# Performance work log

Measured on AMD Instinct MI355X. Metric: run time of the kernel, lower is better.

## Reference

```python
import jax, jax.numpy as jnp
import numpy as np

N = 50000   # nodes
E = 800000  # edges (avg degree 16)
D = 128     # in_channels == num_hidden_channels


def setup_inputs() -> dict:
    key = jax.random.key(0)
    ks = jax.random.split(key, 8)
    embs = jax.random.normal(ks[0], (N, D), dtype=jnp.float32)
    edge_index0 = jax.random.randint(ks[1], (2, E), 0, N)
    edge_index1 = jax.random.randint(ks[2], (2, E), 0, N)
    s = 1.0 / np.sqrt(D)  # torch Linear default init bound
    Wl0 = jax.random.uniform(ks[3], (D, D), jnp.float32, -s, s)
    Wr0 = jax.random.uniform(ks[4], (D, D), jnp.float32, -s, s)
    bl0 = jax.random.uniform(ks[5], (D,), jnp.float32, -s, s)
    Wl1 = jax.random.uniform(ks[6], (D, D), jnp.float32, -s, s)
    Wr1 = jax.random.uniform(ks[7], (D, D), jnp.float32, -s, s)
    bl1 = jnp.zeros((D,), jnp.float32)
    return {"embs": embs, "edge_index0": edge_index0, "edge_index1": edge_index1,
            "Wl0": Wl0, "bl0": bl0, "Wr0": Wr0, "Wl1": Wl1, "bl1": bl1, "Wr1": Wr1}


def sage_conv(x, edge_index, Wl, bl, Wr):
    # PyG SAGEConv, aggr='mean': out = lin_l(mean_{j->i} x_j) + lin_r(x_i)
    src, dst = edge_index[0], edge_index[1]
    msg = x[src]  # [E, D] gather of source-node features
    agg = jax.ops.segment_sum(msg, dst, num_segments=x.shape[0])            # [N, D]
    cnt = jax.ops.segment_sum(jnp.ones((src.shape[0],), x.dtype), dst,
                              num_segments=x.shape[0])                      # [N]
    mean = agg / jnp.maximum(cnt, 1.0)[:, None]  # isolated nodes -> 0 (scatter_mean)
    return mean @ Wl + bl + x @ Wr


def reference(embs, edge_index0, edge_index1, Wl0, bl0, Wr0, Wl1, bl1, Wr1):
    # outer layer 0 (not last) -> conv, dropout (eval: identity), exact GELU
    x = sage_conv(embs, edge_index0, Wl0, bl0, Wr0)
    x = jax.nn.gelu(x, approximate=False)
    # outer layer 1 (last) -> conv only
    x = sage_conv(x, edge_index1, Wl1, bl1, Wr1)
    return x
```

## Files before the change

### kernel.cpp

```cpp
#include <hip/hip_runtime.h>
#include <math.h>

#define D 128
#define BKT_SHIFT 8
#define CHUNK 4096
#define CAP 5120
#define CAPC 56

typedef __attribute__((ext_vector_type(8))) short bf8;
typedef __attribute__((ext_vector_type(4))) float f4;

__device__ __forceinline__ float b2f(ushort u) {
    union { uint i; float f; } x; x.i = ((uint)u) << 16; return x.f;
}
__device__ __forceinline__ ushort f2b(float f) {
    union { float f; uint i; } x; x.f = f;
    uint i = x.i;
    i += 0x7fffu + ((i >> 16) & 1u);
    return (ushort)(i >> 16);
}

__global__ __launch_bounds__(256)
void prep_scatter(const int* __restrict__ ei0, const int* __restrict__ ei1, int E,
                  int ncnk, int* __restrict__ chunkcnt, uint* __restrict__ tmpf,
                  const float* __restrict__ embs, ushort* __restrict__ xb, long n4,
                  const float* __restrict__ Wl0, const float* __restrict__ Wr0,
                  const float* __restrict__ Wl1, const float* __restrict__ Wr1,
                  ushort* __restrict__ WTsw) {
    __shared__ char smem[3088 + CHUNK * 4];
    const int t = threadIdx.x;

    if (blockIdx.y == 2) {
        if (blockIdx.x < 4) {
            const float* Wsrc = blockIdx.x == 0 ? Wl0 : blockIdx.x == 1 ? Wr0
                               : blockIdx.x == 2 ? Wl1 : Wr1;
            ushort* dstm = WTsw + (size_t)blockIdx.x * D * D;
            ushort (*tile)[33] = (ushort(*)[33])smem;
            const int r  = t >> 3;
            const int c0 = (t & 7) * 4;
            for (int tt = 0; tt < 16; ++tt) {
                int ti = tt >> 2, tj = tt & 3;
                float4 v = *(const float4*)(Wsrc + (ti * 32 + r) * D + tj * 32 + c0);
                tile[r][c0 + 0] = f2b(v.x);
                tile[r][c0 + 1] = f2b(v.y);
                tile[r][c0 + 2] = f2b(v.z);
                tile[r][c0 + 3] = f2b(v.w);
                __syncthreads();
                int row = tj * 32 + r;
                int off = row * 256 + (ti * 32 + c0) * 2;
                int doff = off ^ ((row & 7) << 4);
                ushort4 o = { tile[c0 + 0][r], tile[c0 + 1][r],
                              tile[c0 + 2][r], tile[c0 + 3][r] };
                *(ushort4*)((char*)dstm + doff) = o;
                __syncthreads();
            }
            return;
        }
        long i = (long)(blockIdx.x - 4) * 256 + t;
        long stride = (long)(gridDim.x - 4) * 256;
        for (; i < n4; i += stride) {
            float4 v = ((const float4*)embs)[i];
            ushort4 o = { f2b(v.x), f2b(v.y), f2b(v.z), f2b(v.w) };
            ((ushort4*)xb)[i] = o;
        }
        return;
    }

    int* lhist  = (int*)smem;
    int* lstart = (int*)(smem + 1024);
    int* lcur   = (int*)(smem + 2048);
    int* ws     = (int*)(smem + 3072);
    uint* sw    = (uint*)(smem + 3088);
    const int layer = blockIdx.y;
    const int* ei = layer ? ei1 : ei0;
    uint* tp = tmpf + ((size_t)layer * ncnk + blockIdx.x) * 256 * CAPC;
    const int e0 = blockIdx.x * CHUNK;
    const int cnt = min(CHUNK, E - e0);
    lhist[t] = 0;
    __syncthreads();
    for (int i = t; i < cnt; i += 256)
        atomicAdd(&lhist[ei[E + e0 + i] >> BKT_SHIFT], 1);
    __syncthreads();
    {
        int lane = t & 63, wid = t >> 6;
        int v = lhist[t];
        int incl = v;
        #pragma unroll
        for (int o = 1; o < 64; o <<= 1) { int u = __shfl_up(incl, o); if (lane >= o) incl += u; }
        if (lane == 63) ws[wid] = incl;
        __syncthreads();
        int wb = 0;
        #pragma unroll
        for (int w = 0; w < 3; ++w) if (w < wid) wb += ws[w];
        int excl = incl - v + wb;
        lstart[t] = excl;
        lcur[t] = excl;
    }
    __syncthreads();
    for (int i = t; i < cnt; i += 256) {
        int s = ei[e0 + i];
        int d = ei[E + e0 + i];
        int r = atomicAdd(&lcur[d >> BKT_SHIFT], 1);
        sw[r] = ((uint)d << 16) | (uint)s;
    }
    __syncthreads();
    chunkcnt[((size_t)layer * ncnk + blockIdx.x) * 256 + t] = min(lhist[t], CAPC);
    for (int i = t; i < cnt; i += 256) {
        uint w = sw[i];
        int b = w >> 24;
        int o = i - lstart[b];
        if (o < CAPC) tp[b * CAPC + o] = w;
    }
}

__global__ __launch_bounds__(256)
void exact_place(const uint* __restrict__ tmpf, const int* __restrict__ chunkcnt,
                 int ncnk,
                 int* __restrict__ o0, int* __restrict__ o1,
                 int* __restrict__ d0, int* __restrict__ d1,
                 ushort* __restrict__ s0, ushort* __restrict__ s1, int N) {
    const int layer = blockIdx.y;
    const int b = blockIdx.x;
    int* offs = layer ? o1 : o0;
    int* deg  = layer ? d1 : d0;
    ushort* srcs = layer ? s1 : s0;
    __shared__ int lh[256], lc[256], ccnt[256];
    __shared__ int ws[4];
    const int t = threadIdx.x;
    const int lane = t & 63, wid = t >> 6;
    const int node0 = b << BKT_SHIFT;
    const int bstart = b * CAP;

    lh[t] = 0;
    ccnt[t] = (t < ncnk) ? chunkcnt[((size_t)layer * ncnk + t) * 256 + b] : 0;
    __syncthreads();

    for (int c = wid; c < ncnk; c += 4) {
        int cc = ccnt[c];
        if (lane < cc) {
            uint w = tmpf[(((size_t)layer * ncnk + c) * 256 + b) * CAPC + lane];
            atomicAdd(&lh[(w >> 16) & 255], 1);
        }
    }
    __syncthreads();
    {
        int v = lh[t];
        int incl = v;
        #pragma unroll
        for (int o = 1; o < 64; o <<= 1) { int u = __shfl_up(incl, o); if (lane >= o) incl += u; }
        if (lane == 63) ws[wid] = incl;
        __syncthreads();
        int wb = 0;
        #pragma unroll
        for (int w = 0; w < 3; ++w) if (w < wid) wb += ws[w];
        int excl = incl - v + wb;
        int node = node0 + t;
        if (node < N) { offs[node] = bstart + excl; deg[node] = v; }
        lc[t] = bstart + excl;
    }
    __syncthreads();
    for (int c = wid; c < ncnk; c += 4) {
        int cc = ccnt[c];
        if (lane < cc) {
            uint w = tmpf[(((size_t)layer * ncnk + c) * 256 + b) * CAPC + lane];
            int p = atomicAdd(&lc[(w >> 16) & 255], 1);
            srcs[p] = (ushort)(w & 0xffff);
        }
    }
}

__global__ void gather_mean_b(const ushort* __restrict__ xb, const ushort* __restrict__ srcs,
                              const int* __restrict__ offs, const int* __restrict__ deg,
                              ushort* __restrict__ meanb, int N) {
    int node = blockIdx.x * (blockDim.x >> 6) + (threadIdx.x >> 6);
    if (node >= N) return;
    int lane = threadIdx.x & 63;
    int g = lane >> 4;
    int c = (lane & 15) * 8;
    int beg = offs[node], dc = deg[node];
    int end = beg + dc;
    float a[8] = {0.f, 0.f, 0.f, 0.f, 0.f, 0.f, 0.f, 0.f};
    for (int base = beg + g; base < end; base += 16) {
        int i0 = base, i1 = base + 4, i2 = base + 8, i3 = base + 12;
        int s0 = srcs[i0 < end ? i0 : beg];
        int s1 = srcs[i1 < end ? i1 : beg];
        int s2 = srcs[i2 < end ? i2 : beg];
        int s3 = srcs[i3 < end ? i3 : beg];
        float w0 = i0 < end ? 1.f : 0.f;
        float w1 = i1 < end ? 1.f : 0.f;
        float w2 = i2 < end ? 1.f : 0.f;
        float w3 = i3 < end ? 1.f : 0.f;
        bf8 v0 = *(const bf8*)(xb + (long)s0 * D + c);
        bf8 v1 = *(const bf8*)(xb + (long)s1 * D + c);
        bf8 v2 = *(const bf8*)(xb + (long)s2 * D + c);
        bf8 v3 = *(const bf8*)(xb + (long)s3 * D + c);
        #pragma unroll
        for (int q = 0; q < 8; ++q) {
            a[q] = fmaf(w0, b2f((ushort)v0[q]), a[q]);
            a[q] = fmaf(w1, b2f((ushort)v1[q]), a[q]);
            a[q] = fmaf(w2, b2f((ushort)v2[q]), a[q]);
            a[q] = fmaf(w3, b2f((ushort)v3[q]), a[q]);
        }
    }
    #pragma unroll
    for (int q = 0; q < 8; ++q) {
        a[q] += __shfl_xor(a[q], 16);
        a[q] += __shfl_xor(a[q], 32);
    }
    if (g == 0) {
        float inv = dc > 0 ? 1.0f / (float)dc : 0.0f;
        bf8 o;
        #pragma unroll
        for (int q = 0; q < 8; ++q) o[q] = (short)f2b(a[q] * inv);
        *(bf8*)(meanb + (long)node * D + c) = o;
    }
}

template <int ACT>
__global__ __launch_bounds__(256, 2)
void gemm_mfma(const ushort* __restrict__ meanb, const ushort* __restrict__ xb,
               const ushort* __restrict__ WTsw,
               const float* __restrict__ bias, float* __restrict__ outf,
               ushort* __restrict__ outb, int N) {
    __shared__ ushort sW[2 * D * D];
    const int t = threadIdx.x;
    const int lane = t & 63;
    const int wid  = t >> 6;

    {
        const char* src = (const char*)WTsw;
        char* dst = (char*)sW;
        #pragma unroll
        for (int i = 0; i < 16; ++i) {
            int off = i * 4096 + t * 16;
            __builtin_amdgcn_global_load_lds(
                (const __attribute__((address_space(1))) unsigned int*)(src + off),
                (__attribute__((address_space(3))) unsigned int*)(dst + off),
                16, 0, 0);
        }
    }

    const int r0   = blockIdx.x * 128 + wid * 32;
    const int arow = r0 + (lane & 15);
    const int kg   = lane >> 4;
    const bool full = (r0 + 32 <= N);
    bf8 z = {};
    bf8 am[8], ax[8];
    if (full) {
        #pragma unroll
        for (int m = 0; m < 4; ++m) {
            const long a0 = (long)arow * D + kg * 8 + m * 32;
            am[m]   = *(const bf8*)(meanb + a0);
            ax[m]   = *(const bf8*)(xb + a0);
            am[m+4] = *(const bf8*)(meanb + a0 + 16 * D);
            ax[m+4] = *(const bf8*)(xb + a0 + 16 * D);
        }
    } else {
        #pragma unroll
        for (int m = 0; m < 4; ++m) {
            const long a0 = (long)arow * D + kg * 8 + m * 32;
            if (arow < N)      { am[m]   = *(const bf8*)(meanb + a0);
                                 ax[m]   = *(const bf8*)(xb + a0); }
            else               { am[m]   = z; ax[m]   = z; }
            if (arow + 16 < N) { am[m+4] = *(const bf8*)(meanb + a0 + 16 * D);
                                 ax[m+4] = *(const bf8*)(xb + a0 + 16 * D); }
            else               { am[m+4] = z; ax[m+4] = z; }
        }
    }

    const int sxor = (lane & 7) << 4;
    int p[4];
    #pragma unroll
    for (int m = 0; m < 4; ++m)
        p[m] = (lane & 15) * 256 + ((kg * 16 + m * 64) ^ sxor);

    __syncthreads();

    f4 acc0[8], acc1[8];
    #pragma unroll
    for (int n = 0; n < 8; ++n) { acc0[n] = (f4){0.f,0.f,0.f,0.f}; acc1[n] = (f4){0.f,0.f,0.f,0.f}; }

    #pragma unroll
    for (int m = 0; m < 4; ++m) {
        #pragma unroll
        for (int n = 0; n < 8; ++n) {
            bf8 bl = *(const bf8*)((const char*)sW + n * 4096 + p[m]);
            acc0[n] = __builtin_amdgcn_mfma_f32_16x16x32_bf16(am[m],     bl, acc0[n], 0, 0, 0);
            acc1[n] = __builtin_amdgcn_mfma_f32_16x16x32_bf16(am[m + 4], bl, acc1[n], 0, 0, 0);
        }
    }
    #pragma unroll
    for (int m = 0; m < 4; ++m) {
        #pragma unroll
        for (int n = 0; n < 8; ++n) {
            bf8 br = *(const bf8*)((const char*)sW + 32768 + n * 4096 + p[m]);
            acc0[n] = __builtin_amdgcn_mfma_f32_16x16x32_bf16(ax[m],     br, acc0[n], 0, 0, 0);
            acc1[n] = __builtin_amdgcn_mfma_f32_16x16x32_bf16(ax[m + 4], br, acc1[n], 0, 0, 0);
        }
    }

    const int col0  = lane & 15;
    const int orow0 = r0 + kg * 4;
    #pragma unroll
    for (int n = 0; n < 8; ++n) {
        const int col = n * 16 + col0;
        const float b = bias[col];
        #pragma unroll
        for (int r = 0; r < 4; ++r) {
            #pragma unroll
            for (int h = 0; h < 2; ++h) {
                const int row = orow0 + r + h * 16;
                if (!full && row >= N) continue;
                float v = (h ? acc1[n][r] : acc0[n][r]) + b;
                if (ACT) {
                    v = 0.5f * v * (1.0f + erff(v * 0.70710678118654752f));
                    outb[(long)row * D + col] = f2b(v);
                } else {
                    outf[(long)row * D + col] = v;
                }
            }
        }
    }
}

extern "C" void kernel_launch(void* const* d_in, const int* in_sizes, int n_in,
                              void* d_out, int out_size, void* d_ws, size_t ws_size,
                              hipStream_t stream) {
    const float* embs = (const float*)d_in[0];
    const int*   ei0  = (const int*)d_in[1];
    const int*   ei1  = (const int*)d_in[2];
    const float* Wl0  = (const float*)d_in[3];
    const float* bl0  = (const float*)d_in[4];
    const float* Wr0  = (const float*)d_in[5];
    const float* Wl1  = (const float*)d_in[6];
    const float* bl1  = (const float*)d_in[7];
    const float* Wr1  = (const float*)d_in[8];

    const int N = in_sizes[0] / D;
    const int E = in_sizes[1] / 2;
    float* out = (float*)d_out;

    const int nbkt = (N + 255) >> BKT_SHIFT;
    const int ncnk = (E + CHUNK - 1) / CHUNK;

    char* w = (char*)d_ws;
    ushort* xb    = (ushort*)w;  w += (size_t)N * D * 2;
    ushort* meanb = (ushort*)w;  w += (size_t)N * D * 2;
    ushort* WT    = (ushort*)w;  w += (size_t)4 * D * D * 2;
    int* chunkcnt = (int*)w;     w += (size_t)2 * ncnk * 256 * 4;
    int* offs0    = (int*)w;     w += (size_t)N * 4;
    int* offs1    = (int*)w;     w += (size_t)N * 4;
    int* deg0     = (int*)w;     w += (size_t)N * 4;
    int* deg1     = (int*)w;     w += (size_t)N * 4;
    uint* tmpf    = (uint*)w;    w += (size_t)2 * ncnk * 256 * CAPC * 4;
    ushort* srcs0 = (ushort*)w;  w += (size_t)256 * CAP * 2;
    ushort* srcs1 = (ushort*)w;

    const int ab = (N + 3) / 4;
    const int gb = (N + 127) / 128;

    prep_scatter<<<dim3(ncnk, 3), 256, 0, stream>>>(ei0, ei1, E, ncnk, chunkcnt, tmpf,
                                                    embs, xb, (long)N * D / 4,
                                                    Wl0, Wr0, Wl1, Wr1, WT);
    exact_place<<<dim3(nbkt, 2), 256, 0, stream>>>(tmpf, chunkcnt, ncnk,
                                                   offs0, offs1, deg0, deg1,
                                                   srcs0, srcs1, N);

    gather_mean_b<<<ab, 256, 0, stream>>>(xb, srcs0, offs0, deg0, meanb, N);
    gemm_mfma<1><<<gb, 256, 0, stream>>>(meanb, xb, WT, bl0, nullptr, xb, N);

    gather_mean_b<<<ab, 256, 0, stream>>>(xb, srcs1, offs1, deg1, meanb, N);
    gemm_mfma<0><<<gb, 256, 0, stream>>>(meanb, xb, WT + 2 * D * D, bl1, out, nullptr, N);
}
```

Before: 154.5 us.

## Fuse neighbor-mean gather into MFMA GEMM and make bucket staging contiguous

The separate gather-mean and GEMM kernels are merged into one kernel per layer. Each 1024-thread block builds a 64-row mean tile in swizzled LDS, then runs the mean and self GEMMs with MFMA, reloading the two weight halves into the same LDS buffer one after the other. This removes the meanb round-trip through global memory and two launches, and layer-1 output now goes to a separate buffer instead of overwriting xb in place. The tmpf staging layout is reordered to bucket-major so exact_place reads each bucket's chunks contiguously with all threads. The cost is less GEMM reuse per block (64 rows, more blocks reloading weights) and an extra barrier and weight reload inside each block.

```diff
diff --git a/kernel.cpp b/kernel.cpp
--- a/kernel.cpp
+++ b/kernel.cpp
@@ -73,7 +73,7 @@
     uint* sw    = (uint*)(smem + 3088);
     const int layer = blockIdx.y;
     const int* ei = layer ? ei1 : ei0;
-    uint* tp = tmpf + ((size_t)layer * ncnk + blockIdx.x) * 256 * CAPC;
+    uint* tbase = tmpf + (size_t)layer * 256 * ncnk * CAPC;
     const int e0 = blockIdx.x * CHUNK;
     const int cnt = min(CHUNK, E - e0);
     lhist[t] = 0;
@@ -109,7 +109,8 @@
         uint w = sw[i];
         int b = w >> 24;
         int o = i - lstart[b];
-        if (o < CAPC) tp[b * CAPC + o] = w;
+        if (o < CAPC)
+            tbase[((size_t)b * ncnk + blockIdx.x) * CAPC + o] = w;
     }
 }
 
@@ -124,21 +125,23 @@
     int* offs = layer ? o1 : o0;
     int* deg  = layer ? d1 : d0;
     ushort* srcs = layer ? s1 : s0;
+    const uint* tp = tmpf + ((size_t)layer * 256 + b) * ncnk * CAPC;
     __shared__ int lh[256], lc[256], ccnt[256];
     __shared__ int ws[4];
     const int t = threadIdx.x;
     const int lane = t & 63, wid = t >> 6;
     const int node0 = b << BKT_SHIFT;
     const int bstart = b * CAP;
+    const int total = ncnk * CAPC;
 
     lh[t] = 0;
     ccnt[t] = (t < ncnk) ? chunkcnt[((size_t)layer * ncnk + t) * 256 + b] : 0;
     __syncthreads();
 
-    for (int c = wid; c < ncnk; c += 4) {
-        int cc = ccnt[c];
-        if (lane < cc) {
-            uint w = tmpf[(((size_t)layer * ncnk + c) * 256 + b) * CAPC + lane];
+    for (int i = t; i < total; i += 256) {
+        int c = i / CAPC, s = i - c * CAPC;
+        if (s < ccnt[c]) {
+            uint w = tp[i];
             atomicAdd(&lh[(w >> 16) & 255], 1);
         }
     }
@@ -159,165 +162,144 @@
         lc[t] = bstart + excl;
     }
     __syncthreads();
-    for (int c = wid; c < ncnk; c += 4) {
-        int cc = ccnt[c];
-        if (lane < cc) {
-            uint w = tmpf[(((size_t)layer * ncnk + c) * 256 + b) * CAPC + lane];
+    for (int i = t; i < total; i += 256) {
+        int c = i / CAPC, s = i - c * CAPC;
+        if (s < ccnt[c]) {
+            uint w = tp[i];
             int p = atomicAdd(&lc[(w >> 16) & 255], 1);
             srcs[p] = (ushort)(w & 0xffff);
         }
     }
 }
 
-__global__ void gather_mean_b(const ushort* __restrict__ xb, const ushort* __restrict__ srcs,
-                              const int* __restrict__ offs, const int* __restrict__ deg,
-                              ushort* __restrict__ meanb, int N) {
-    int node = blockIdx.x * (blockDim.x >> 6) + (threadIdx.x >> 6);
-    if (node >= N) return;
-    int lane = threadIdx.x & 63;
-    int g = lane >> 4;
-    int c = (lane & 15) * 8;
-    int beg = offs[node], dc = deg[node];
-    int end = beg + dc;
-    float a[8] = {0.f, 0.f, 0.f, 0.f, 0.f, 0.f, 0.f, 0.f};
-    for (int base = beg + g; base < end; base += 16) {
-        int i0 = base, i1 = base + 4, i2 = base + 8, i3 = base + 12;
-        int s0 = srcs[i0 < end ? i0 : beg];
-        int s1 = srcs[i1 < end ? i1 : beg];
-        int s2 = srcs[i2 < end ? i2 : beg];
-        int s3 = srcs[i3 < end ? i3 : beg];
-        float w0 = i0 < end ? 1.f : 0.f;
-        float w1 = i1 < end ? 1.f : 0.f;
-        float w2 = i2 < end ? 1.f : 0.f;
-        float w3 = i3 < end ? 1.f : 0.f;
-        bf8 v0 = *(const bf8*)(xb + (long)s0 * D + c);
-        bf8 v1 = *(const bf8*)(xb + (long)s1 * D + c);
-        bf8 v2 = *(const bf8*)(xb + (long)s2 * D + c);
-        bf8 v3 = *(const bf8*)(xb + (long)s3 * D + c);
-        #pragma unroll
-        for (int q = 0; q < 8; ++q) {
-            a[q] = fmaf(w0, b2f((ushort)v0[q]), a[q]);
-            a[q] = fmaf(w1, b2f((ushort)v1[q]), a[q]);
-            a[q] = fmaf(w2, b2f((ushort)v2[q]), a[q]);
-            a[q] = fmaf(w3, b2f((ushort)v3[q]), a[q]);
-        }
-    }
-    #pragma unroll
-    for (int q = 0; q < 8; ++q) {
-        a[q] += __shfl_xor(a[q], 16);
-        a[q] += __shfl_xor(a[q], 32);
-    }
-    if (g == 0) {
-        float inv = dc > 0 ? 1.0f / (float)dc : 0.0f;
-        bf8 o;
-        #pragma unroll
-        for (int q = 0; q < 8; ++q) o[q] = (short)f2b(a[q] * inv);
-        *(bf8*)(meanb + (long)node * D + c) = o;
-    }
-}
-
 template <int ACT>
-__global__ __launch_bounds__(256, 2)
-void gemm_mfma(const ushort* __restrict__ meanb, const ushort* __restrict__ xb,
-               const ushort* __restrict__ WTsw,
-               const float* __restrict__ bias, float* __restrict__ outf,
-               ushort* __restrict__ outb, int N) {
-    __shared__ ushort sW[2 * D * D];
+__global__ __launch_bounds__(1024, 8)
+void gather_gemm(const ushort* __restrict__ xin, const ushort* __restrict__ srcs,
+                 const int* __restrict__ offs, const int* __restrict__ deg,
+                 const ushort* __restrict__ WTsw,
+                 const float* __restrict__ bias, float* __restrict__ outf,
+                 ushort* __restrict__ outb, int N) {
+    __shared__ ushort sW[D * D];
+    __shared__ ushort smean[64 * D];
     const int t = threadIdx.x;
     const int lane = t & 63;
-    const int wid  = t >> 6;
-
-    {
-        const char* src = (const char*)WTsw;
-        char* dst = (char*)sW;
-        #pragma unroll
-        for (int i = 0; i < 16; ++i) {
-            int off = i * 4096 + t * 16;
-            __builtin_amdgcn_global_load_lds(
-                (const __attribute__((address_space(1))) unsigned int*)(src + off),
-                (__attribute__((address_space(3))) unsigned int*)(dst + off),
-                16, 0, 0);
-        }
-    }
-
-    const int r0   = blockIdx.x * 128 + wid * 32;
-    const int arow = r0 + (lane & 15);
-    const int kg   = lane >> 4;
-    const bool full = (r0 + 32 <= N);
+    const int w = t >> 6;
+    const int base = blockIdx.x * 64;
+
+    #pragma unroll
+    for (int i = 0; i < 2; ++i) {
+        int off = i * 16384 + t * 16;
+        __builtin_amdgcn_global_load_lds(
+            (const __attribute__((address_space(1))) unsigned int*)((const char*)WTsw + 32768 + off),
+            (__attribute__((address_space(3))) unsigned int*)((char*)sW + off), 16, 0, 0);
+    }
+
+    const int g = lane >> 4;
+    const int c8 = (lane & 15) * 8;
+    for (int j = 0; j < 4; ++j) {
+        const int rl = w * 4 + j;
+        const int node = base + rl;
+        float a[8] = {0.f,0.f,0.f,0.f,0.f,0.f,0.f,0.f};
+        int dc = 0;
+        if (node < N) {
+            int beg = offs[node]; dc = deg[node];
+            int end = beg + dc;
+            for (int bb = beg + g; bb < end; bb += 16) {
+                int i0 = bb, i1 = bb + 4, i2 = bb + 8, i3 = bb + 12;
+                int s0 = srcs[i0 < end ? i0 : beg];
+                int s1 = srcs[i1 < end ? i1 : beg];
+                int s2 = srcs[i2 < end ? i2 : beg];
+                int s3 = srcs[i3 < end ? i3 : beg];
+                float w0 = i0 < end ? 1.f : 0.f;
+                float w1 = i1 < end ? 1.f : 0.f;
+                float w2 = i2 < end ? 1.f : 0.f;
+                float w3 = i3 < end ? 1.f : 0.f;
+                bf8 v0 = *(const bf8*)(xin + (long)s0 * D + c8);
+                bf8 v1 = *(const bf8*)(xin + (long)s1 * D + c8);
+                bf8 v2 = *(const bf8*)(xin + (long)s2 * D + c8);
+                bf8 v3 = *(const bf8*)(xin + (long)s3 * D + c8);
+                #pragma unroll
+                for (int q = 0; q < 8; ++q) {
+                    a[q] = fmaf(w0, b2f((ushort)v0[q]), a[q]);
+                    a[q] = fmaf(w1, b2f((ushort)v1[q]), a[q]);
+                    a[q] = fmaf(w2, b2f((ushort)v2[q]), a[q]);
+                    a[q] = fmaf(w3, b2f((ushort)v3[q]), a[q]);
+                }
+            }
+            #pragma unroll
+            for (int q = 0; q < 8; ++q) {
+                a[q] += __shfl_xor(a[q], 16);
+                a[q] += __shfl_xor(a[q], 32);
+            }
+        }
+        if (g == 0) {
+            float inv = dc > 0 ? 1.0f / (float)dc : 0.0f;
+            bf8 o;
+            #pragma unroll
+            for (int q = 0; q < 8; ++q) o[q] = (short)f2b(a[q] * inv);
+            int byte = rl * 256 + (lane & 15) * 16;
+            byte ^= (rl & 7) << 4;
+            *(bf8*)((char*)smean + byte) = o;
+        }
+    }
+    __syncthreads();
+
+    const int tm = w >> 2;
+    const int q  = w & 3;
+    const int l15 = lane & 15, kg = lane >> 4;
+    const int sx = (lane & 7) << 4;
+    const int arl = tm * 16 + l15;
+    const int xrow = base + arl;
+    const int n0 = q * 2;
+    f4 acc0 = {0.f,0.f,0.f,0.f}, acc1 = {0.f,0.f,0.f,0.f};
     bf8 z = {};
-    bf8 am[8], ax[8];
-    if (full) {
-        #pragma unroll
-        for (int m = 0; m < 4; ++m) {
-            const long a0 = (long)arow * D + kg * 8 + m * 32;
-            am[m]   = *(const bf8*)(meanb + a0);
-            ax[m]   = *(const bf8*)(xb + a0);
-            am[m+4] = *(const bf8*)(meanb + a0 + 16 * D);
-            ax[m+4] = *(const bf8*)(xb + a0 + 16 * D);
-        }
-    } else {
-        #pragma unroll
-        for (int m = 0; m < 4; ++m) {
-            const long a0 = (long)arow * D + kg * 8 + m * 32;
-            if (arow < N)      { am[m]   = *(const bf8*)(meanb + a0);
-                                 ax[m]   = *(const bf8*)(xb + a0); }
-            else               { am[m]   = z; ax[m]   = z; }
-            if (arow + 16 < N) { am[m+4] = *(const bf8*)(meanb + a0 + 16 * D);
-                                 ax[m+4] = *(const bf8*)(xb + a0 + 16 * D); }
-            else               { am[m+4] = z; ax[m+4] = z; }
-        }
-    }
-
-    const int sxor = (lane & 7) << 4;
-    int p[4];
-    #pragma unroll
-    for (int m = 0; m < 4; ++m)
-        p[m] = (lane & 15) * 256 + ((kg * 16 + m * 64) ^ sxor);
-
-    __syncthreads();
-
-    f4 acc0[8], acc1[8];
-    #pragma unroll
-    for (int n = 0; n < 8; ++n) { acc0[n] = (f4){0.f,0.f,0.f,0.f}; acc1[n] = (f4){0.f,0.f,0.f,0.f}; }
 
     #pragma unroll
     for (int m = 0; m < 4; ++m) {
-        #pragma unroll
-        for (int n = 0; n < 8; ++n) {
-            bf8 bl = *(const bf8*)((const char*)sW + n * 4096 + p[m]);
-            acc0[n] = __builtin_amdgcn_mfma_f32_16x16x32_bf16(am[m],     bl, acc0[n], 0, 0, 0);
-            acc1[n] = __builtin_amdgcn_mfma_f32_16x16x32_bf16(am[m + 4], bl, acc1[n], 0, 0, 0);
-        }
-    }
+        int ksw = (kg * 16 + m * 64) ^ sx;
+        bf8 ax = z;
+        if (xrow < N) ax = *(const bf8*)(xin + (long)xrow * D + kg * 8 + m * 32);
+        bf8 b0 = *(const bf8*)((const char*)sW + n0 * 4096 + l15 * 256 + ksw);
+        bf8 b1 = *(const bf8*)((const char*)sW + (n0 + 1) * 4096 + l15 * 256 + ksw);
+        acc0 = __builtin_amdgcn_mfma_f32_16x16x32_bf16(ax, b0, acc0, 0, 0, 0);
+        acc1 = __builtin_amdgcn_mfma_f32_16x16x32_bf16(ax, b1, acc1, 0, 0, 0);
+    }
+    __syncthreads();
+
+    #pragma unroll
+    for (int i = 0; i < 2; ++i) {
+        int off = i * 16384 + t * 16;
+        __builtin_amdgcn_global_load_lds(
+            (const __attribute__((address_space(1))) unsigned int*)((const char*)WTsw + off),
+            (__attribute__((address_space(3))) unsigned int*)((char*)sW + off), 16, 0, 0);
+    }
+    __syncthreads();
+
     #pragma unroll
     for (int m = 0; m < 4; ++m) {
-        #pragma unroll
-        for (int n = 0; n < 8; ++n) {
-            bf8 br = *(const bf8*)((const char*)sW + 32768 + n * 4096 + p[m]);
-            acc0[n] = __builtin_amdgcn_mfma_f32_16x16x32_bf16(ax[m],     br, acc0[n], 0, 0, 0);
-            acc1[n] = __builtin_amdgcn_mfma_f32_16x16x32_bf16(ax[m + 4], br, acc1[n], 0, 0, 0);
-        }
-    }
-
-    const int col0  = lane & 15;
-    const int orow0 = r0 + kg * 4;
-    #pragma unroll
-    for (int n = 0; n < 8; ++n) {
-        const int col = n * 16 + col0;
-        const float b = bias[col];
+        int ksw = (kg * 16 + m * 64) ^ sx;
+        bf8 al = *(const bf8*)((const char*)smean + arl * 256 + ksw);
+        bf8 b0 = *(const bf8*)((const char*)sW + n0 * 4096 + l15 * 256 + ksw);
+        bf8 b1 = *(const bf8*)((const char*)sW + (n0 + 1) * 4096 + l15 * 256 + ksw);
+        acc0 = __builtin_amdgcn_mfma_f32_16x16x32_bf16(al, b0, acc0, 0, 0, 0);
+        acc1 = __builtin_amdgcn_mfma_f32_16x16x32_bf16(al, b1, acc1, 0, 0, 0);
+    }
+
+    #pragma unroll
+    for (int nn = 0; nn < 2; ++nn) {
+        const int col = (n0 + nn) * 16 + l15;
+        const float bb = bias[col];
+        f4 av = nn ? acc1 : acc0;
         #pragma unroll
         for (int r = 0; r < 4; ++r) {
-            #pragma unroll
-            for (int h = 0; h < 2; ++h) {
-                const int row = orow0 + r + h * 16;
-                if (!full && row >= N) continue;
-                float v = (h ? acc1[n][r] : acc0[n][r]) + b;
-                if (ACT) {
-                    v = 0.5f * v * (1.0f + erff(v * 0.70710678118654752f));
-                    outb[(long)row * D + col] = f2b(v);
-                } else {
-                    outf[(long)row * D + col] = v;
-                }
+            const int row = base + tm * 16 + kg * 4 + r;
+            if (row >= N) continue;
+            float v = av[r] + bb;
+            if (ACT) {
+                v = 0.5f * v * (1.0f + erff(v * 0.70710678118654752f));
+                outb[(long)row * D + col] = f2b(v);
+            } else {
+                outf[(long)row * D + col] = v;
             }
         }
     }
@@ -345,19 +327,18 @@
 
     char* w = (char*)d_ws;
     ushort* xb    = (ushort*)w;  w += (size_t)N * D * 2;
-    ushort* meanb = (ushort*)w;  w += (size_t)N * D * 2;
+    ushort* x1b   = (ushort*)w;  w += (size_t)N * D * 2;
     ushort* WT    = (ushort*)w;  w += (size_t)4 * D * D * 2;
     int* chunkcnt = (int*)w;     w += (size_t)2 * ncnk * 256 * 4;
     int* offs0    = (int*)w;     w += (size_t)N * 4;
     int* offs1    = (int*)w;     w += (size_t)N * 4;
     int* deg0     = (int*)w;     w += (size_t)N * 4;
     int* deg1     = (int*)w;     w += (size_t)N * 4;
-    uint* tmpf    = (uint*)w;    w += (size_t)2 * ncnk * 256 * CAPC * 4;
+    uint* tmpf    = (uint*)w;    w += (size_t)2 * 256 * ncnk * CAPC * 4;
     ushort* srcs0 = (ushort*)w;  w += (size_t)256 * CAP * 2;
     ushort* srcs1 = (ushort*)w;
 
-    const int ab = (N + 3) / 4;
-    const int gb = (N + 127) / 128;
+    const int gb = (N + 63) / 64;
 
     prep_scatter<<<dim3(ncnk, 3), 256, 0, stream>>>(ei0, ei1, E, ncnk, chunkcnt, tmpf,
                                                     embs, xb, (long)N * D / 4,
@@ -366,9 +347,8 @@
                                                    offs0, offs1, deg0, deg1,
                                                    srcs0, srcs1, N);
 
-    gather_mean_b<<<ab, 256, 0, stream>>>(xb, srcs0, offs0, deg0, meanb, N);
-    gemm_mfma<1><<<gb, 256, 0, stream>>>(meanb, xb, WT, bl0, nullptr, xb, N);
-
-    gather_mean_b<<<ab, 256, 0, stream>>>(xb, srcs1, offs1, deg1, meanb, N);
-    gemm_mfma<0><<<gb, 256, 0, stream>>>(meanb, xb, WT + 2 * D * D, bl1, out, nullptr, N);
-}
+    gather_gemm<1><<<gb, 1024, 0, stream>>>(xb, srcs0, offs0, deg0, WT, bl0,
+                                            nullptr, x1b, N);
+    gather_gemm<0><<<gb, 1024, 0, stream>>>(x1b, srcs1, offs1, deg1, WT + 2 * D * D,
+                                            bl1, out, nullptr, N);
+}
```

After: 143.7 us. 1.08x faster.

## Transpose bucket staging layout and preload neighbor indices via wave shuffles

Applied to the files above, without the earlier changes.

The staging buffer is reordered from chunk-major to bucket-major, so each exact_place block reads its bucket's entries from one contiguous span with all threads striding linearly. Before, each wave read short per-chunk segments. The gather kernel now loads up to 64 neighbor indices per node in a single coalesced read and hands them out with __shfl, instead of issuing four dependent index loads per iteration. Nodes with more than 64 neighbors fall back to a scalar loop. The contiguous scan adds an integer divide per element and also reads slots past each chunk's count, which are then masked out.

```diff
diff --git a/kernel.cpp b/kernel.cpp
--- a/kernel.cpp
+++ b/kernel.cpp
@@ -73,7 +73,7 @@
     uint* sw    = (uint*)(smem + 3088);
     const int layer = blockIdx.y;
     const int* ei = layer ? ei1 : ei0;
-    uint* tp = tmpf + ((size_t)layer * ncnk + blockIdx.x) * 256 * CAPC;
+    uint* tbase = tmpf + (size_t)layer * 256 * ncnk * CAPC;
     const int e0 = blockIdx.x * CHUNK;
     const int cnt = min(CHUNK, E - e0);
     lhist[t] = 0;
@@ -109,7 +109,8 @@
         uint w = sw[i];
         int b = w >> 24;
         int o = i - lstart[b];
-        if (o < CAPC) tp[b * CAPC + o] = w;
+        if (o < CAPC)
+            tbase[((size_t)b * ncnk + blockIdx.x) * CAPC + o] = w;
     }
 }
 
@@ -124,21 +125,23 @@
     int* offs = layer ? o1 : o0;
     int* deg  = layer ? d1 : d0;
     ushort* srcs = layer ? s1 : s0;
+    const uint* tp = tmpf + ((size_t)layer * 256 + b) * ncnk * CAPC;
     __shared__ int lh[256], lc[256], ccnt[256];
     __shared__ int ws[4];
     const int t = threadIdx.x;
     const int lane = t & 63, wid = t >> 6;
     const int node0 = b << BKT_SHIFT;
     const int bstart = b * CAP;
+    const int total = ncnk * CAPC;
 
     lh[t] = 0;
     ccnt[t] = (t < ncnk) ? chunkcnt[((size_t)layer * ncnk + t) * 256 + b] : 0;
     __syncthreads();
 
-    for (int c = wid; c < ncnk; c += 4) {
-        int cc = ccnt[c];
-        if (lane < cc) {
-            uint w = tmpf[(((size_t)layer * ncnk + c) * 256 + b) * CAPC + lane];
+    for (int i = t; i < total; i += 256) {
+        int c = i / CAPC, s = i - c * CAPC;
+        if (s < ccnt[c]) {
+            uint w = tp[i];
             atomicAdd(&lh[(w >> 16) & 255], 1);
         }
     }
@@ -159,37 +162,40 @@
         lc[t] = bstart + excl;
     }
     __syncthreads();
-    for (int c = wid; c < ncnk; c += 4) {
-        int cc = ccnt[c];
-        if (lane < cc) {
-            uint w = tmpf[(((size_t)layer * ncnk + c) * 256 + b) * CAPC + lane];
+    for (int i = t; i < total; i += 256) {
+        int c = i / CAPC, s = i - c * CAPC;
+        if (s < ccnt[c]) {
+            uint w = tp[i];
             int p = atomicAdd(&lc[(w >> 16) & 255], 1);
             srcs[p] = (ushort)(w & 0xffff);
         }
     }
 }
 
-__global__ void gather_mean_b(const ushort* __restrict__ xb, const ushort* __restrict__ srcs,
-                              const int* __restrict__ offs, const int* __restrict__ deg,
-                              ushort* __restrict__ meanb, int N) {
-    int node = blockIdx.x * (blockDim.x >> 6) + (threadIdx.x >> 6);
+__global__ __launch_bounds__(256)
+void gather_mean_b(const ushort* __restrict__ xb, const ushort* __restrict__ srcs,
+                   const int* __restrict__ offs, const int* __restrict__ deg,
+                   ushort* __restrict__ meanb, int N) {
+    int node = blockIdx.x * 4 + (threadIdx.x >> 6);
     if (node >= N) return;
     int lane = threadIdx.x & 63;
     int g = lane >> 4;
     int c = (lane & 15) * 8;
     int beg = offs[node], dc = deg[node];
-    int end = beg + dc;
-    float a[8] = {0.f, 0.f, 0.f, 0.f, 0.f, 0.f, 0.f, 0.f};
-    for (int base = beg + g; base < end; base += 16) {
-        int i0 = base, i1 = base + 4, i2 = base + 8, i3 = base + 12;
-        int s0 = srcs[i0 < end ? i0 : beg];
-        int s1 = srcs[i1 < end ? i1 : beg];
-        int s2 = srcs[i2 < end ? i2 : beg];
-        int s3 = srcs[i3 < end ? i3 : beg];
-        float w0 = i0 < end ? 1.f : 0.f;
-        float w1 = i1 < end ? 1.f : 0.f;
-        float w2 = i2 < end ? 1.f : 0.f;
-        float w3 = i3 < end ? 1.f : 0.f;
+    int si = 0;
+    if (lane < dc) si = srcs[beg + lane];
+    float a[8] = {0.f,0.f,0.f,0.f,0.f,0.f,0.f,0.f};
+    const int cap = dc < 64 ? dc : 64;
+    for (int kb = 0; kb < cap; kb += 16) {
+        int i0 = kb + g, i1 = i0 + 4, i2 = i0 + 8, i3 = i0 + 12;
+        int s0 = __shfl(si, i0);
+        int s1 = __shfl(si, i1);
+        int s2 = __shfl(si, i2);
+        int s3 = __shfl(si, i3);
+        float w0 = i0 < dc ? 1.f : 0.f;
+        float w1 = i1 < dc ? 1.f : 0.f;
+        float w2 = i2 < dc ? 1.f : 0.f;
+        float w3 = i3 < dc ? 1.f : 0.f;
         bf8 v0 = *(const bf8*)(xb + (long)s0 * D + c);
         bf8 v1 = *(const bf8*)(xb + (long)s1 * D + c);
         bf8 v2 = *(const bf8*)(xb + (long)s2 * D + c);
@@ -201,6 +207,12 @@
             a[q] = fmaf(w2, b2f((ushort)v2[q]), a[q]);
             a[q] = fmaf(w3, b2f((ushort)v3[q]), a[q]);
         }
+    }
+    for (int e = beg + 64 + g; e < beg + dc; e += 4) {
+        int s = srcs[e];
+        bf8 v = *(const bf8*)(xb + (long)s * D + c);
+        #pragma unroll
+        for (int q = 0; q < 8; ++q) a[q] += b2f((ushort)v[q]);
     }
     #pragma unroll
     for (int q = 0; q < 8; ++q) {
@@ -352,7 +364,7 @@
     int* offs1    = (int*)w;     w += (size_t)N * 4;
     int* deg0     = (int*)w;     w += (size_t)N * 4;
     int* deg1     = (int*)w;     w += (size_t)N * 4;
-    uint* tmpf    = (uint*)w;    w += (size_t)2 * ncnk * 256 * CAPC * 4;
+    uint* tmpf    = (uint*)w;    w += (size_t)2 * 256 * ncnk * CAPC * 4;
     ushort* srcs0 = (ushort*)w;  w += (size_t)256 * CAP * 2;
     ushort* srcs1 = (ushort*)w;
 
```

New measurement: 148.7 us. 1.04x faster.
